# Performance work log

Hardware: AMD Instinct MI355X
Metric: run time of the kernel (lower is better)

## Reference

```python
import jax, jax.numpy as jnp
import numpy as np

B, S, D = 2, 2048, 1024
H = 16
HD = D // H  # head_dim = 64
NEG = -1e30  # finite stand-in for -inf; masked entries are zeroed after softmax so math matches


def setup_inputs() -> dict:
    key = jax.random.key(0)
    ks = jax.random.split(key, 10)
    q = jax.random.normal(ks[0], (B, S, D), dtype=jnp.float32)
    k = jax.random.normal(ks[1], (B, S, D), dtype=jnp.float32)
    v = jax.random.normal(ks[2], (B, S, D), dtype=jnp.float32)
    mask = jax.random.randint(ks[3], (B, S), 0, 2).astype(bool)
    s = 1.0 / np.sqrt(D)
    Wq = jax.random.uniform(ks[4], (D, D), jnp.float32, -s, s)
    bq = jax.random.uniform(ks[5], (D,), jnp.float32, -s, s)
    Wk = jax.random.uniform(ks[6], (D, D), jnp.float32, -s, s)
    bk = jax.random.uniform(ks[7], (D,), jnp.float32, -s, s)
    Wv = jax.random.uniform(ks[8], (D, D), jnp.float32, -s, s)
    bv = jax.random.uniform(ks[9], (D,), jnp.float32, -s, s)
    return {"q": q, "k": k, "v": v, "mask": mask,
            "Wq": Wq, "bq": bq, "Wk": Wk, "bk": bk, "Wv": Wv, "bv": bv}


def _split_heads(x):
    # [B,S,D] -> [H,B,S,HD]  (matches permute(2,0,1,3) in torch)
    return x.reshape(B, S, H, HD).transpose(2, 0, 1, 3)


def reference(q, k, v, mask, Wq, bq, Wk, bk, Wv, bv):
    mq = _split_heads(q @ Wq.T + bq)
    mk = _split_heads(k @ Wk.T + bk)
    mv = _split_heads(v @ Wv.T + bv)
    # scores: [H,B,Sq,Sk]
    scores = jnp.einsum('hbqd,hbkd->hbqk', mq, mk) / jnp.sqrt(jnp.float32(HD))
    pair_mask = (mask[:, :, None] & mask[:, None, :])[None]  # [1,B,S,S]
    scores = jnp.where(pair_mask, scores, NEG)
    attn = jax.nn.softmax(scores, axis=-1)
    attn = jnp.where(pair_mask, attn, 0.0)
    out = jnp.einsum('hbqk,hbkd->hbqd', attn, mv)
    # [H,B,S,HD] -> [B,S,D]
    return out.transpose(1, 2, 0, 3).reshape(B, S, H * HD)
```

## Files before the change

### kernel.cpp

```cpp
#include <hip/hip_runtime.h>
#include <math.h>

#define B_ 2
#define S_ 2048
#define D_ 1024
#define H_ 16
#define HD_ 64

typedef __bf16 bf16_t;
typedef bf16_t bf16x8 __attribute__((ext_vector_type(8)));
typedef bf16_t bf16x4v __attribute__((ext_vector_type(4)));
typedef float f32x4 __attribute__((ext_vector_type(4)));

#define GLOBAL_LOAD_LDS16(gp, lp)                                              \
    __builtin_amdgcn_global_load_lds(                                          \
        (const __attribute__((address_space(1))) void*)(gp),                   \
        (__attribute__((address_space(3))) void*)(lp), 16, 0, 0)

__global__ __launch_bounds__(256) void cvt_kernel(
    const float* __restrict__ q, const float* __restrict__ k,
    const float* __restrict__ v, const float* __restrict__ wq,
    const float* __restrict__ wk, const float* __restrict__ wv,
    bf16_t* __restrict__ qb, bf16_t* __restrict__ kb, bf16_t* __restrict__ vb,
    bf16_t* __restrict__ wqb, bf16_t* __restrict__ wkb, bf16_t* __restrict__ wvb)
{
    const int y = blockIdx.y;
    const float* src;
    bf16_t* dst;
    size_t n;
    switch (y) {
        case 0: src = q;  dst = qb;  n = (size_t)B_ * S_ * D_; break;
        case 1: src = k;  dst = kb;  n = (size_t)B_ * S_ * D_; break;
        case 2: src = v;  dst = vb;  n = (size_t)B_ * S_ * D_; break;
        case 3: src = wq; dst = wqb; n = (size_t)D_ * D_;      break;
        case 4: src = wk; dst = wkb; n = (size_t)D_ * D_;      break;
        default: src = wv; dst = wvb; n = (size_t)D_ * D_;     break;
    }
    size_t idx = ((size_t)blockIdx.x * 256 + threadIdx.x) * 4;
    if (idx >= n) return;
    float4 f = *(const float4*)(src + idx);
    bf16x4v o;
    o[0] = (bf16_t)f.x; o[1] = (bf16_t)f.y;
    o[2] = (bf16_t)f.z; o[3] = (bf16_t)f.w;
    *(bf16x4v*)(dst + idx) = o;
}

__global__ __launch_bounds__(256) void proj_mfma(
    const bf16_t* __restrict__ X0, const bf16_t* __restrict__ X1,
    const bf16_t* __restrict__ X2, const bf16_t* __restrict__ W0,
    const bf16_t* __restrict__ W1, const bf16_t* __restrict__ W2,
    const float* __restrict__ b0, const float* __restrict__ b1,
    const float* __restrict__ b2, bf16_t* __restrict__ o0,
    bf16_t* __restrict__ o1, bf16_t* __restrict__ o2)
{
    __shared__ __align__(16) bf16_t As[128 * 32];
    __shared__ __align__(16) bf16_t Bs[128 * 32];

    const int z = blockIdx.z;
    const bf16_t* X = (z == 0) ? X0 : (z == 1) ? X1 : X2;
    const bf16_t* W = (z == 0) ? W0 : (z == 1) ? W1 : W2;
    const float* bias = (z == 0) ? b0 : (z == 1) ? b1 : b2;
    bf16_t* out = (z == 0) ? o0 : (z == 1) ? o1 : o2;
    const float oscale = (z == 0) ? 0.125f : 1.0f;

    const int tid  = threadIdx.x;
    const int w    = tid >> 6;
    const int lane = tid & 63;
    const int L    = lane & 15;
    const int quad = lane >> 4;
    const int wr   = (w >> 1) * 64;
    const int wc   = (w & 1) * 64;
    const int row0 = blockIdx.x * 128;
    const int col0 = blockIdx.y * 128;

    const int lr = lane >> 2;
    const int lc = (lane & 3) * 8;

    f32x4 acc[4][4];
    #pragma unroll
    for (int i = 0; i < 4; ++i)
        #pragma unroll
        for (int j = 0; j < 4; ++j) {
            acc[i][j][0] = 0.f; acc[i][j][1] = 0.f;
            acc[i][j][2] = 0.f; acc[i][j][3] = 0.f;
        }

    for (int k0 = 0; k0 < D_; k0 += 32) {
        __syncthreads();
        #pragma unroll
        for (int i = 0; i < 2; ++i) {
            const int rA = i * 64 + w * 16;
            GLOBAL_LOAD_LDS16(X + (size_t)(row0 + rA + lr) * D_ + k0 + lc,
                              &As[rA * 32]);
            GLOBAL_LOAD_LDS16(W + (size_t)(col0 + rA + lr) * D_ + k0 + lc,
                              &Bs[rA * 32]);
        }
        __syncthreads();

        bf16x8 aF[4], bF[4];
        #pragma unroll
        for (int t = 0; t < 4; ++t) {
            aF[t] = *(const bf16x8*)&As[(wr + t * 16 + L) * 32 + quad * 8];
            bF[t] = *(const bf16x8*)&Bs[(wc + t * 16 + L) * 32 + quad * 8];
        }
        #pragma unroll
        for (int mt = 0; mt < 4; ++mt)
            #pragma unroll
            for (int nt = 0; nt < 4; ++nt)
                acc[mt][nt] = __builtin_amdgcn_mfma_f32_16x16x32_bf16(
                    aF[mt], bF[nt], acc[mt][nt], 0, 0, 0);
    }

    #pragma unroll
    for (int nt = 0; nt < 4; ++nt) {
        const int j  = col0 + wc + nt * 16 + L;
        const float bval = bias[j];
        const int h  = j >> 6;
        const int hd = j & 63;
        #pragma unroll
        for (int mt = 0; mt < 4; ++mt)
            #pragma unroll
            for (int r = 0; r < 4; ++r) {
                const int n = row0 + wr + mt * 16 + quad * 4 + r;
                const int b = n >> 11;
                const int s = n & (S_ - 1);
                out[((((size_t)b * H_ + h) * S_ + s) * HD_) + hd] =
                    (bf16_t)((acc[mt][nt][r] + bval) * oscale);
            }
    }
}

__global__ __launch_bounds__(256) void transpose_v(
    const bf16_t* __restrict__ mv, bf16_t* __restrict__ vt)
{
    __shared__ bf16_t tile[64][72];
    const int s0 = blockIdx.x * 64;
    const int bh = blockIdx.y;
    const int t  = threadIdx.x;

    const bf16_t* src = mv + ((size_t)bh * S_ + s0) * HD_;
    {
        int srow = t >> 2, c16 = (t & 3) * 16;
        bf16x8 a = *(const bf16x8*)(src + srow * HD_ + c16);
        bf16x8 b = *(const bf16x8*)(src + srow * HD_ + c16 + 8);
        *(bf16x8*)&tile[srow][c16]     = a;
        *(bf16x8*)&tile[srow][c16 + 8] = b;
    }
    __syncthreads();

    const int d  = t & 63;
    const int sc = (t >> 6) * 16;
    unsigned int w[8];
    #pragma unroll
    for (int j = 0; j < 8; ++j) {
        unsigned short lo = *(const unsigned short*)&tile[sc + 2*j][d];
        unsigned short hi = *(const unsigned short*)&tile[sc + 2*j + 1][d];
        w[j] = (unsigned int)lo | ((unsigned int)hi << 16);
    }
    bf16_t* dst = vt + ((size_t)bh * HD_ + d) * S_ + s0 + sc;
    uint4 u0; u0.x = w[0]; u0.y = w[1]; u0.z = w[2]; u0.w = w[3];
    uint4 u1; u1.x = w[4]; u1.y = w[5]; u1.z = w[6]; u1.w = w[7];
    ((uint4*)dst)[0] = u0;
    ((uint4*)dst)[1] = u1;
}

__global__ __launch_bounds__(256) void attn_kernel(
    const bf16_t* __restrict__ Q, const bf16_t* __restrict__ K,
    const bf16_t* __restrict__ Vt, const int* __restrict__ mask,
    float* __restrict__ out)
{
    constexpr int LD = 72;
    __shared__ bf16_t Ks[64 * LD];
    __shared__ bf16_t Vs[64 * LD];
    __shared__ bf16_t Pt[4][32 * LD];
    __shared__ float  kvb[64];

    const int tid  = threadIdx.x;
    const int w    = tid >> 6;
    const int lane = tid & 63;
    const int L    = lane & 15;
    const int quad = lane >> 4;
    const int h    = blockIdx.y;
    const int b    = blockIdx.z;
    const int bh   = b * H_ + h;
    const int q0   = blockIdx.x * 128;

    const bf16_t* kbase = K  + (size_t)bh * S_ * HD_;
    const bf16_t* vbase = Vt + (size_t)bh * HD_ * S_;
    const int*    mrow  = mask + b * S_;

    bf16x8 aQ[2][2];
    #pragma unroll
    for (int qb = 0; qb < 2; ++qb) {
        const bf16_t* qp = Q + ((size_t)bh * S_ + q0 + w * 32 + qb * 16 + L) * HD_;
        aQ[qb][0] = *(const bf16x8*)(qp + quad * 8);
        aQ[qb][1] = *(const bf16x8*)(qp + 32 + quad * 8);
    }

    f32x4 o[2][4];
    #pragma unroll
    for (int qb = 0; qb < 2; ++qb)
        #pragma unroll
        for (int f = 0; f < 4; ++f) {
            o[qb][f][0]=0.f; o[qb][f][1]=0.f; o[qb][f][2]=0.f; o[qb][f][3]=0.f;
        }
    float l_[2] = {0.f, 0.f};

    for (int kt = 0; kt < S_; kt += 64) {
        __syncthreads();
        for (int i = tid; i < 512; i += 256) {
            int r = i >> 3, c = (i & 7) * 8;
            *(bf16x8*)&Ks[r * LD + c] =
                *(const bf16x8*)(kbase + (size_t)(kt + r) * HD_ + c);
            *(bf16x8*)&Vs[r * LD + c] =
                *(const bf16x8*)(vbase + (size_t)r * S_ + kt + c);
        }
        if (tid < 64) kvb[tid] = mrow[kt + tid] ? -8.0f : -1e30f;
        __syncthreads();

        bf16x8 aK[4][2];
        f32x4  bias[4];
        #pragma unroll
        for (int f = 0; f < 4; ++f) {
            aK[f][0] = *(const bf16x8*)&Ks[(f * 16 + L) * LD + quad * 8];
            aK[f][1] = *(const bf16x8*)&Ks[(f * 16 + L) * LD + 32 + quad * 8];
            bias[f]  = *(const f32x4*)&kvb[f * 16 + quad * 4];
        }

        bf16_t* pw = &Pt[w][0];
        #pragma unroll
        for (int qb = 0; qb < 2; ++qb) {
            #pragma unroll
            for (int f = 0; f < 4; ++f) {
                f32x4 z = bias[f];
                z = __builtin_amdgcn_mfma_f32_16x16x32_bf16(aK[f][0], aQ[qb][0], z, 0, 0, 0);
                z = __builtin_amdgcn_mfma_f32_16x16x32_bf16(aK[f][1], aQ[qb][1], z, 0, 0, 0);
                bf16x4v p4;
                float s0_ = __expf(z[0]);
                float s1_ = __expf(z[1]);
                float s2_ = __expf(z[2]);
                float s3_ = __expf(z[3]);
                p4[0] = (bf16_t)s0_; p4[1] = (bf16_t)s1_;
                p4[2] = (bf16_t)s2_; p4[3] = (bf16_t)s3_;
                l_[qb] += (s0_ + s1_) + (s2_ + s3_);
                *(bf16x4v*)&pw[(qb * 16 + L) * LD + f * 16 + quad * 4] = p4;
            }
        }

        bf16x8 aP[2][2];
        #pragma unroll
        for (int qb = 0; qb < 2; ++qb) {
            aP[qb][0] = *(const bf16x8*)&pw[(qb * 16 + L) * LD + quad * 8];
            aP[qb][1] = *(const bf16x8*)&pw[(qb * 16 + L) * LD + 32 + quad * 8];
        }

        #pragma unroll
        for (int f = 0; f < 4; ++f) {
            bf16x8 bV0 = *(const bf16x8*)&Vs[(f * 16 + L) * LD + quad * 8];
            bf16x8 bV1 = *(const bf16x8*)&Vs[(f * 16 + L) * LD + 32 + quad * 8];
            #pragma unroll
            for (int qb = 0; qb < 2; ++qb) {
                o[qb][f] = __builtin_amdgcn_mfma_f32_16x16x32_bf16(aP[qb][0], bV0, o[qb][f], 0, 0, 0);
                o[qb][f] = __builtin_amdgcn_mfma_f32_16x16x32_bf16(aP[qb][1], bV1, o[qb][f], 0, 0, 0);
            }
        }
    }

    #pragma unroll
    for (int qb = 0; qb < 2; ++qb) {
        float t = l_[qb];
        t += __shfl_xor(t, 16);
        t += __shfl_xor(t, 32);
        int qv = mrow[q0 + w * 32 + qb * 16 + L];
        l_[qb] = (qv && t > 0.f) ? (1.0f / t) : 0.0f;
    }

    #pragma unroll
    for (int qb = 0; qb < 2; ++qb) {
        float inv[4];
        #pragma unroll
        for (int r = 0; r < 4; ++r)
            inv[r] = __shfl(l_[qb], quad * 4 + r);
        float* obase = out + ((size_t)b * S_ + q0 + w * 32 + qb * 16 + quad * 4) * D_ + h * HD_;
        #pragma unroll
        for (int f = 0; f < 4; ++f)
            #pragma unroll
            for (int r = 0; r < 4; ++r)
                obase[r * D_ + f * 16 + L] = o[qb][f][r] * inv[r];
    }
}

extern "C" void kernel_launch(void* const* d_in, const int* in_sizes, int n_in,
                              void* d_out, int out_size, void* d_ws, size_t ws_size,
                              hipStream_t stream)
{
    const float* q    = (const float*)d_in[0];
    const float* k    = (const float*)d_in[1];
    const float* v    = (const float*)d_in[2];
    const int*   mask = (const int*)d_in[3];
    const float* Wq   = (const float*)d_in[4];
    const float* bq   = (const float*)d_in[5];
    const float* Wk   = (const float*)d_in[6];
    const float* bk   = (const float*)d_in[7];
    const float* Wv   = (const float*)d_in[8];
    const float* bv   = (const float*)d_in[9];
    float* out = (float*)d_out;

    const size_t PE = (size_t)B_ * S_ * D_;
    const size_t WE = (size_t)D_ * D_;

    bf16_t* qb  = (bf16_t*)d_ws;
    bf16_t* kb  = qb + PE;
    bf16_t* vb  = kb + PE;
    bf16_t* wqb = vb + PE;
    bf16_t* wkb = wqb + WE;
    bf16_t* wvb = wkb + WE;
    bf16_t* mq  = wvb + WE;
    bf16_t* mk  = mq + PE;
    bf16_t* mv  = mk + PE;
    bf16_t* vt  = mv + PE;

    dim3 cgrid(PE / (256 * 4), 6);
    cvt_kernel<<<cgrid, 256, 0, stream>>>(q, k, v, Wq, Wk, Wv,
                                          qb, kb, vb, wqb, wkb, wvb);

    dim3 pgrid(4096 / 128, 1024 / 128, 3);
    proj_mfma<<<pgrid, 256, 0, stream>>>(qb, kb, vb, wqb, wkb, wvb,
                                         bq, bk, bv, mq, mk, mv);

    dim3 tgrid(S_ / 64, B_ * H_);
    transpose_v<<<tgrid, 256, 0, stream>>>(mv, vt);

    dim3 agrid(S_ / 128, H_, B_);
    attn_kernel<<<agrid, 256, 0, stream>>>(mq, mk, vt, mask, out);
}
```

Baseline: 223.6 us.

## Load K/V fragments directly from global in attention, drop LDS staging

The attention kernel stops staging K and V tiles in shared memory behind two barriers per step. Each wave now loads its MFMA fragments straight from global/L2, and each block covers 64 queries instead of 128, which doubles the grid and raises occupancy (launch bounds 256,4). The mask-to-bias conversion moves into the conversion kernel as a precomputed float array. Halving queries per block doubles total K/V global traffic, and the uncoalesced per-lane fragment loads lean on the caches.

```diff
diff --git a/kernel.cpp b/kernel.cpp
--- a/kernel.cpp
+++ b/kernel.cpp
@@ -21,10 +21,26 @@
     const float* __restrict__ q, const float* __restrict__ k,
     const float* __restrict__ v, const float* __restrict__ wq,
     const float* __restrict__ wk, const float* __restrict__ wv,
+    const int* __restrict__ msk,
     bf16_t* __restrict__ qb, bf16_t* __restrict__ kb, bf16_t* __restrict__ vb,
-    bf16_t* __restrict__ wqb, bf16_t* __restrict__ wkb, bf16_t* __restrict__ wvb)
+    bf16_t* __restrict__ wqb, bf16_t* __restrict__ wkb, bf16_t* __restrict__ wvb,
+    float* __restrict__ kbias)
 {
     const int y = blockIdx.y;
+    size_t idx = ((size_t)blockIdx.x * 256 + threadIdx.x) * 4;
+
+    if (y == 6) {
+        if (idx >= (size_t)B_ * S_) return;
+        int4 mi = *(const int4*)(msk + idx);
+        float4 o4;
+        o4.x = mi.x ? -8.0f : -1e30f;
+        o4.y = mi.y ? -8.0f : -1e30f;
+        o4.z = mi.z ? -8.0f : -1e30f;
+        o4.w = mi.w ? -8.0f : -1e30f;
+        *(float4*)(kbias + idx) = o4;
+        return;
+    }
+
     const float* src;
     bf16_t* dst;
     size_t n;
@@ -36,7 +52,6 @@
         case 4: src = wk; dst = wkb; n = (size_t)D_ * D_;      break;
         default: src = wv; dst = wvb; n = (size_t)D_ * D_;     break;
     }
-    size_t idx = ((size_t)blockIdx.x * 256 + threadIdx.x) * 4;
     if (idx >= n) return;
     float4 f = *(const float4*)(src + idx);
     bf16x4v o;
@@ -164,16 +179,13 @@
     ((uint4*)dst)[1] = u1;
 }
 
-__global__ __launch_bounds__(256) void attn_kernel(
+__global__ __launch_bounds__(256, 4) void attn_kernel(
     const bf16_t* __restrict__ Q, const bf16_t* __restrict__ K,
-    const bf16_t* __restrict__ Vt, const int* __restrict__ mask,
-    float* __restrict__ out)
-{
-    constexpr int LD = 72;
-    __shared__ bf16_t Ks[64 * LD];
-    __shared__ bf16_t Vs[64 * LD];
-    __shared__ bf16_t Pt[4][32 * LD];
-    __shared__ float  kvb[64];
+    const bf16_t* __restrict__ Vt, const float* __restrict__ kbias,
+    const int* __restrict__ mask, float* __restrict__ out)
+{
+    constexpr int LDP = 72;
+    __shared__ bf16_t Pt[4][16 * LDP];
 
     const int tid  = threadIdx.x;
     const int w    = tid >> 6;
@@ -183,111 +195,91 @@
     const int h    = blockIdx.y;
     const int b    = blockIdx.z;
     const int bh   = b * H_ + h;
-    const int q0   = blockIdx.x * 128;
+    const int q0   = blockIdx.x * 64;
+    const int qrow = q0 + w * 16 + L;
 
     const bf16_t* kbase = K  + (size_t)bh * S_ * HD_;
     const bf16_t* vbase = Vt + (size_t)bh * HD_ * S_;
-    const int*    mrow  = mask + b * S_;
-
-    bf16x8 aQ[2][2];
-    #pragma unroll
-    for (int qb = 0; qb < 2; ++qb) {
-        const bf16_t* qp = Q + ((size_t)bh * S_ + q0 + w * 32 + qb * 16 + L) * HD_;
-        aQ[qb][0] = *(const bf16x8*)(qp + quad * 8);
-        aQ[qb][1] = *(const bf16x8*)(qp + 32 + quad * 8);
-    }
-
-    f32x4 o[2][4];
-    #pragma unroll
-    for (int qb = 0; qb < 2; ++qb)
-        #pragma unroll
-        for (int f = 0; f < 4; ++f) {
-            o[qb][f][0]=0.f; o[qb][f][1]=0.f; o[qb][f][2]=0.f; o[qb][f][3]=0.f;
-        }
-    float l_[2] = {0.f, 0.f};
+    const float*  bbase = kbias + b * S_;
+
+    const bf16_t* qp = Q + ((size_t)bh * S_ + qrow) * HD_;
+    const bf16x8 aQ0 = *(const bf16x8*)(qp + quad * 8);
+    const bf16x8 aQ1 = *(const bf16x8*)(qp + 32 + quad * 8);
+
+    f32x4 o[4];
+    #pragma unroll
+    for (int f = 0; f < 4; ++f) { o[f][0]=0.f; o[f][1]=0.f; o[f][2]=0.f; o[f][3]=0.f; }
+    float l_ = 0.f;
+
+    bf16_t* pw = &Pt[w][0];
 
     for (int kt = 0; kt < S_; kt += 64) {
-        __syncthreads();
-        for (int i = tid; i < 512; i += 256) {
-            int r = i >> 3, c = (i & 7) * 8;
-            *(bf16x8*)&Ks[r * LD + c] =
-                *(const bf16x8*)(kbase + (size_t)(kt + r) * HD_ + c);
-            *(bf16x8*)&Vs[r * LD + c] =
-                *(const bf16x8*)(vbase + (size_t)r * S_ + kt + c);
-        }
-        if (tid < 64) kvb[tid] = mrow[kt + tid] ? -8.0f : -1e30f;
-        __syncthreads();
-
-        bf16x8 aK[4][2];
-        f32x4  bias[4];
-        #pragma unroll
-        for (int f = 0; f < 4; ++f) {
-            aK[f][0] = *(const bf16x8*)&Ks[(f * 16 + L) * LD + quad * 8];
-            aK[f][1] = *(const bf16x8*)&Ks[(f * 16 + L) * LD + 32 + quad * 8];
-            bias[f]  = *(const f32x4*)&kvb[f * 16 + quad * 4];
-        }
-
-        bf16_t* pw = &Pt[w][0];
-        #pragma unroll
-        for (int qb = 0; qb < 2; ++qb) {
+        f32x4 sc[4];
+        {
+            bf16x8 aK[4][2];
             #pragma unroll
             for (int f = 0; f < 4; ++f) {
-                f32x4 z = bias[f];
-                z = __builtin_amdgcn_mfma_f32_16x16x32_bf16(aK[f][0], aQ[qb][0], z, 0, 0, 0);
-                z = __builtin_amdgcn_mfma_f32_16x16x32_bf16(aK[f][1], aQ[qb][1], z, 0, 0, 0);
-                bf16x4v p4;
-                float s0_ = __expf(z[0]);
-                float s1_ = __expf(z[1]);
-                float s2_ = __expf(z[2]);
-                float s3_ = __expf(z[3]);
-                p4[0] = (bf16_t)s0_; p4[1] = (bf16_t)s1_;
-                p4[2] = (bf16_t)s2_; p4[3] = (bf16_t)s3_;
-                l_[qb] += (s0_ + s1_) + (s2_ + s3_);
-                *(bf16x4v*)&pw[(qb * 16 + L) * LD + f * 16 + quad * 4] = p4;
+                const bf16_t* kp = kbase + (size_t)(kt + f * 16 + L) * HD_;
+                aK[f][0] = *(const bf16x8*)(kp + quad * 8);
+                aK[f][1] = *(const bf16x8*)(kp + 32 + quad * 8);
             }
-        }
-
-        bf16x8 aP[2][2];
-        #pragma unroll
-        for (int qb = 0; qb < 2; ++qb) {
-            aP[qb][0] = *(const bf16x8*)&pw[(qb * 16 + L) * LD + quad * 8];
-            aP[qb][1] = *(const bf16x8*)&pw[(qb * 16 + L) * LD + 32 + quad * 8];
-        }
-
+            #pragma unroll
+            for (int f = 0; f < 4; ++f) {
+                f32x4 z = *(const f32x4*)(bbase + kt + f * 16 + quad * 4);
+                z = __builtin_amdgcn_mfma_f32_16x16x32_bf16(aK[f][0], aQ0, z, 0, 0, 0);
+                z = __builtin_amdgcn_mfma_f32_16x16x32_bf16(aK[f][1], aQ1, z, 0, 0, 0);
+                sc[f] = z;
+            }
+        }
+
+        bf16x8 bV[4][2];
         #pragma unroll
         for (int f = 0; f < 4; ++f) {
-            bf16x8 bV0 = *(const bf16x8*)&Vs[(f * 16 + L) * LD + quad * 8];
-            bf16x8 bV1 = *(const bf16x8*)&Vs[(f * 16 + L) * LD + 32 + quad * 8];
-            #pragma unroll
-            for (int qb = 0; qb < 2; ++qb) {
-                o[qb][f] = __builtin_amdgcn_mfma_f32_16x16x32_bf16(aP[qb][0], bV0, o[qb][f], 0, 0, 0);
-                o[qb][f] = __builtin_amdgcn_mfma_f32_16x16x32_bf16(aP[qb][1], bV1, o[qb][f], 0, 0, 0);
-            }
-        }
-    }
-
-    #pragma unroll
-    for (int qb = 0; qb < 2; ++qb) {
-        float t = l_[qb];
-        t += __shfl_xor(t, 16);
-        t += __shfl_xor(t, 32);
-        int qv = mrow[q0 + w * 32 + qb * 16 + L];
-        l_[qb] = (qv && t > 0.f) ? (1.0f / t) : 0.0f;
-    }
-
-    #pragma unroll
-    for (int qb = 0; qb < 2; ++qb) {
-        float inv[4];
+            const bf16_t* vp = vbase + (size_t)(f * 16 + L) * S_ + kt;
+            bV[f][0] = *(const bf16x8*)(vp + quad * 8);
+            bV[f][1] = *(const bf16x8*)(vp + 32 + quad * 8);
+        }
+
+        #pragma unroll
+        for (int f = 0; f < 4; ++f) {
+            float e0 = __expf(sc[f][0]);
+            float e1 = __expf(sc[f][1]);
+            float e2 = __expf(sc[f][2]);
+            float e3 = __expf(sc[f][3]);
+            l_ += (e0 + e1) + (e2 + e3);
+            bf16x4v p4;
+            p4[0] = (bf16_t)e0; p4[1] = (bf16_t)e1;
+            p4[2] = (bf16_t)e2; p4[3] = (bf16_t)e3;
+            *(bf16x4v*)&pw[L * LDP + f * 16 + quad * 4] = p4;
+        }
+
+        bf16x8 aP0 = *(const bf16x8*)&pw[L * LDP + quad * 8];
+        bf16x8 aP1 = *(const bf16x8*)&pw[L * LDP + 32 + quad * 8];
+
+        #pragma unroll
+        for (int f = 0; f < 4; ++f) {
+            o[f] = __builtin_amdgcn_mfma_f32_16x16x32_bf16(aP0, bV[f][0], o[f], 0, 0, 0);
+            o[f] = __builtin_amdgcn_mfma_f32_16x16x32_bf16(aP1, bV[f][1], o[f], 0, 0, 0);
+        }
+    }
+
+    float t = l_;
+    t += __shfl_xor(t, 16);
+    t += __shfl_xor(t, 32);
+    int qv = mask[b * S_ + qrow];
+    float linv = (qv && t > 0.f) ? (1.0f / t) : 0.0f;
+
+    float inv[4];
+    #pragma unroll
+    for (int r = 0; r < 4; ++r)
+        inv[r] = __shfl(linv, quad * 4 + r);
+
+    float* obase = out + ((size_t)b * S_ + q0 + w * 16 + quad * 4) * D_ + h * HD_;
+    #pragma unroll
+    for (int f = 0; f < 4; ++f)
         #pragma unroll
         for (int r = 0; r < 4; ++r)
-            inv[r] = __shfl(l_[qb], quad * 4 + r);
-        float* obase = out + ((size_t)b * S_ + q0 + w * 32 + qb * 16 + quad * 4) * D_ + h * HD_;
-        #pragma unroll
-        for (int f = 0; f < 4; ++f)
-            #pragma unroll
-            for (int r = 0; r < 4; ++r)
-                obase[r * D_ + f * 16 + L] = o[qb][f][r] * inv[r];
-    }
+            obase[r * D_ + f * 16 + L] = o[f][r] * inv[r];
 }
 
 extern "C" void kernel_launch(void* const* d_in, const int* in_sizes, int n_in,
@@ -309,20 +301,21 @@
     const size_t PE = (size_t)B_ * S_ * D_;
     const size_t WE = (size_t)D_ * D_;
 
-    bf16_t* qb  = (bf16_t*)d_ws;
-    bf16_t* kb  = qb + PE;
-    bf16_t* vb  = kb + PE;
-    bf16_t* wqb = vb + PE;
-    bf16_t* wkb = wqb + WE;
-    bf16_t* wvb = wkb + WE;
-    bf16_t* mq  = wvb + WE;
-    bf16_t* mk  = mq + PE;
-    bf16_t* mv  = mk + PE;
-    bf16_t* vt  = mv + PE;
-
-    dim3 cgrid(PE / (256 * 4), 6);
-    cvt_kernel<<<cgrid, 256, 0, stream>>>(q, k, v, Wq, Wk, Wv,
-                                          qb, kb, vb, wqb, wkb, wvb);
+    bf16_t* qb    = (bf16_t*)d_ws;
+    bf16_t* kb    = qb + PE;
+    bf16_t* vb    = kb + PE;
+    bf16_t* wqb   = vb + PE;
+    bf16_t* wkb   = wqb + WE;
+    bf16_t* wvb   = wkb + WE;
+    bf16_t* mq    = wvb + WE;
+    bf16_t* mk    = mq + PE;
+    bf16_t* mv    = mk + PE;
+    bf16_t* vt    = mv + PE;
+    float*  kbias = (float*)(vt + PE);
+
+    dim3 cgrid(PE / (256 * 4), 7);
+    cvt_kernel<<<cgrid, 256, 0, stream>>>(q, k, v, Wq, Wk, Wv, mask,
+                                          qb, kb, vb, wqb, wkb, wvb, kbias);
 
     dim3 pgrid(4096 / 128, 1024 / 128, 3);
     proj_mfma<<<pgrid, 256, 0, stream>>>(qb, kb, vb, wqb, wkb, wvb,
@@ -331,6 +324,6 @@
     dim3 tgrid(S_ / 64, B_ * H_);
     transpose_v<<<tgrid, 256, 0, stream>>>(mv, vt);
 
-    dim3 agrid(S_ / 128, H_, B_);
-    attn_kernel<<<agrid, 256, 0, stream>>>(mq, mk, vt, mask, out);
-}
+    dim3 agrid(S_ / 64, H_, B_);
+    attn_kernel<<<agrid, 256, 0, stream>>>(mq, mk, vt, kbias, mask, out);
+}
```

Result: slower. 396.2 us (+77.2%).

## Register-prefetch next K/V tile and precompute key mask bias in conversion kernel

Applied to the files above, without the earlier changes.

The attention loop now loads the next 64-key K and V^T tiles, plus the per-key bias, into registers while the current tile is being computed, then stores them to shared memory at the top of the next iteration. This replaces the synchronous global-to-LDS copy. The mask-to-bias conversion (-8 or -1e30) moves into an extra grid row of the conversion kernel, so the attention kernel reads precomputed floats and drops its shared kvb array. The cost is more register pressure from the prefetch buffers and an extra workspace buffer.

```diff
diff --git a/kernel.cpp b/kernel.cpp
--- a/kernel.cpp
+++ b/kernel.cpp
@@ -21,10 +21,26 @@
     const float* __restrict__ q, const float* __restrict__ k,
     const float* __restrict__ v, const float* __restrict__ wq,
     const float* __restrict__ wk, const float* __restrict__ wv,
+    const int* __restrict__ msk,
     bf16_t* __restrict__ qb, bf16_t* __restrict__ kb, bf16_t* __restrict__ vb,
-    bf16_t* __restrict__ wqb, bf16_t* __restrict__ wkb, bf16_t* __restrict__ wvb)
+    bf16_t* __restrict__ wqb, bf16_t* __restrict__ wkb, bf16_t* __restrict__ wvb,
+    float* __restrict__ kbias)
 {
     const int y = blockIdx.y;
+    size_t idx = ((size_t)blockIdx.x * 256 + threadIdx.x) * 4;
+
+    if (y == 6) {
+        if (idx >= (size_t)B_ * S_) return;
+        int4 mi = *(const int4*)(msk + idx);
+        float4 o4;
+        o4.x = mi.x ? -8.0f : -1e30f;
+        o4.y = mi.y ? -8.0f : -1e30f;
+        o4.z = mi.z ? -8.0f : -1e30f;
+        o4.w = mi.w ? -8.0f : -1e30f;
+        *(float4*)(kbias + idx) = o4;
+        return;
+    }
+
     const float* src;
     bf16_t* dst;
     size_t n;
@@ -36,7 +52,6 @@
         case 4: src = wk; dst = wkb; n = (size_t)D_ * D_;      break;
         default: src = wv; dst = wvb; n = (size_t)D_ * D_;     break;
     }
-    size_t idx = ((size_t)blockIdx.x * 256 + threadIdx.x) * 4;
     if (idx >= n) return;
     float4 f = *(const float4*)(src + idx);
     bf16x4v o;
@@ -166,14 +181,13 @@
 
 __global__ __launch_bounds__(256) void attn_kernel(
     const bf16_t* __restrict__ Q, const bf16_t* __restrict__ K,
-    const bf16_t* __restrict__ Vt, const int* __restrict__ mask,
-    float* __restrict__ out)
+    const bf16_t* __restrict__ Vt, const float* __restrict__ kbias,
+    const int* __restrict__ mask, float* __restrict__ out)
 {
     constexpr int LD = 72;
     __shared__ bf16_t Ks[64 * LD];
     __shared__ bf16_t Vs[64 * LD];
     __shared__ bf16_t Pt[4][32 * LD];
-    __shared__ float  kvb[64];
 
     const int tid  = threadIdx.x;
     const int w    = tid >> 6;
@@ -187,7 +201,11 @@
 
     const bf16_t* kbase = K  + (size_t)bh * S_ * HD_;
     const bf16_t* vbase = Vt + (size_t)bh * HD_ * S_;
+    const float*  bbase = kbias + b * S_;
     const int*    mrow  = mask + b * S_;
+
+    const int sr = tid >> 3;
+    const int sc2 = (tid & 7) * 8;
 
     bf16x8 aQ[2][2];
     #pragma unroll
@@ -206,25 +224,45 @@
         }
     float l_[2] = {0.f, 0.f};
 
+    bf16x8 kr0, kr1, vr0, vr1;
+    f32x4  bias_n[4];
+    {
+        kr0 = *(const bf16x8*)(kbase + (size_t)sr * HD_ + sc2);
+        kr1 = *(const bf16x8*)(kbase + (size_t)(sr + 32) * HD_ + sc2);
+        vr0 = *(const bf16x8*)(vbase + (size_t)sr * S_ + sc2);
+        vr1 = *(const bf16x8*)(vbase + (size_t)(sr + 32) * S_ + sc2);
+        #pragma unroll
+        for (int f = 0; f < 4; ++f)
+            bias_n[f] = *(const f32x4*)(bbase + f * 16 + quad * 4);
+    }
+
     for (int kt = 0; kt < S_; kt += 64) {
         __syncthreads();
-        for (int i = tid; i < 512; i += 256) {
-            int r = i >> 3, c = (i & 7) * 8;
-            *(bf16x8*)&Ks[r * LD + c] =
-                *(const bf16x8*)(kbase + (size_t)(kt + r) * HD_ + c);
-            *(bf16x8*)&Vs[r * LD + c] =
-                *(const bf16x8*)(vbase + (size_t)r * S_ + kt + c);
-        }
-        if (tid < 64) kvb[tid] = mrow[kt + tid] ? -8.0f : -1e30f;
+        *(bf16x8*)&Ks[sr * LD + sc2]        = kr0;
+        *(bf16x8*)&Ks[(sr + 32) * LD + sc2] = kr1;
+        *(bf16x8*)&Vs[sr * LD + sc2]        = vr0;
+        *(bf16x8*)&Vs[(sr + 32) * LD + sc2] = vr1;
+        f32x4 bias_c[4];
+        #pragma unroll
+        for (int f = 0; f < 4; ++f) bias_c[f] = bias_n[f];
         __syncthreads();
 
+        if (kt + 64 < S_) {
+            const int kn = kt + 64;
+            kr0 = *(const bf16x8*)(kbase + (size_t)(kn + sr) * HD_ + sc2);
+            kr1 = *(const bf16x8*)(kbase + (size_t)(kn + sr + 32) * HD_ + sc2);
+            vr0 = *(const bf16x8*)(vbase + (size_t)sr * S_ + kn + sc2);
+            vr1 = *(const bf16x8*)(vbase + (size_t)(sr + 32) * S_ + kn + sc2);
+            #pragma unroll
+            for (int f = 0; f < 4; ++f)
+                bias_n[f] = *(const f32x4*)(bbase + kn + f * 16 + quad * 4);
+        }
+
         bf16x8 aK[4][2];
-        f32x4  bias[4];
         #pragma unroll
         for (int f = 0; f < 4; ++f) {
             aK[f][0] = *(const bf16x8*)&Ks[(f * 16 + L) * LD + quad * 8];
             aK[f][1] = *(const bf16x8*)&Ks[(f * 16 + L) * LD + 32 + quad * 8];
-            bias[f]  = *(const f32x4*)&kvb[f * 16 + quad * 4];
         }
 
         bf16_t* pw = &Pt[w][0];
@@ -232,17 +270,17 @@
         for (int qb = 0; qb < 2; ++qb) {
             #pragma unroll
             for (int f = 0; f < 4; ++f) {
-                f32x4 z = bias[f];
+                f32x4 z = bias_c[f];
                 z = __builtin_amdgcn_mfma_f32_16x16x32_bf16(aK[f][0], aQ[qb][0], z, 0, 0, 0);
                 z = __builtin_amdgcn_mfma_f32_16x16x32_bf16(aK[f][1], aQ[qb][1], z, 0, 0, 0);
+                float e0 = __expf(z[0]);
+                float e1 = __expf(z[1]);
+                float e2 = __expf(z[2]);
+                float e3 = __expf(z[3]);
+                l_[qb] += (e0 + e1) + (e2 + e3);
                 bf16x4v p4;
-                float s0_ = __expf(z[0]);
-                float s1_ = __expf(z[1]);
-                float s2_ = __expf(z[2]);
-                float s3_ = __expf(z[3]);
-                p4[0] = (bf16_t)s0_; p4[1] = (bf16_t)s1_;
-                p4[2] = (bf16_t)s2_; p4[3] = (bf16_t)s3_;
-                l_[qb] += (s0_ + s1_) + (s2_ + s3_);
+                p4[0] = (bf16_t)e0; p4[1] = (bf16_t)e1;
+                p4[2] = (bf16_t)e2; p4[3] = (bf16_t)e3;
                 *(bf16x4v*)&pw[(qb * 16 + L) * LD + f * 16 + quad * 4] = p4;
             }
         }
@@ -309,20 +347,21 @@
     const size_t PE = (size_t)B_ * S_ * D_;
     const size_t WE = (size_t)D_ * D_;
 
-    bf16_t* qb  = (bf16_t*)d_ws;
-    bf16_t* kb  = qb + PE;
-    bf16_t* vb  = kb + PE;
-    bf16_t* wqb = vb + PE;
-    bf16_t* wkb = wqb + WE;
-    bf16_t* wvb = wkb + WE;
-    bf16_t* mq  = wvb + WE;
-    bf16_t* mk  = mq + PE;
-    bf16_t* mv  = mk + PE;
-    bf16_t* vt  = mv + PE;
-
-    dim3 cgrid(PE / (256 * 4), 6);
-    cvt_kernel<<<cgrid, 256, 0, stream>>>(q, k, v, Wq, Wk, Wv,
-                                          qb, kb, vb, wqb, wkb, wvb);
+    bf16_t* qb    = (bf16_t*)d_ws;
+    bf16_t* kb    = qb + PE;
+    bf16_t* vb    = kb + PE;
+    bf16_t* wqb   = vb + PE;
+    bf16_t* wkb   = wqb + WE;
+    bf16_t* wvb   = wkb + WE;
+    bf16_t* mq    = wvb + WE;
+    bf16_t* mk    = mq + PE;
+    bf16_t* mv    = mk + PE;
+    bf16_t* vt    = mv + PE;
+    float*  kbias = (float*)(vt + PE);
+
+    dim3 cgrid(PE / (256 * 4), 7);
+    cvt_kernel<<<cgrid, 256, 0, stream>>>(q, k, v, Wq, Wk, Wv, mask,
+                                          qb, kb, vb, wqb, wkb, wvb, kbias);
 
     dim3 pgrid(4096 / 128, 1024 / 128, 3);
     proj_mfma<<<pgrid, 256, 0, stream>>>(qb, kb, vb, wqb, wkb, wvb,
@@ -332,5 +371,5 @@
     transpose_v<<<tgrid, 256, 0, stream>>>(mv, vt);
 
     dim3 agrid(S_ / 128, H_, B_);
-    attn_kernel<<<agrid, 256, 0, stream>>>(mq, mk, vt, mask, out);
-}
+    attn_kernel<<<agrid, 256, 0, stream>>>(mq, mk, vt, kbias, mask, out);
+}
```

Result: faster. 211.6 us (-5.4%).
